# Kernel optimization log

Measured on AMD Instinct MI355X. Metric: run time of the kernel, lower is better.

## Reference

```python
import jax, jax.numpy as jnp
import numpy as np

N = 40000
E = 640000
IN_C = 128
HID = 256
HEADS = 8


def _gat(x, W, att_src, att_dst, bias, src, dst, num_nodes, heads, concat):
    # x: [N, Fin], W: [Fin, heads*C], att_*: [heads, C], bias: [out_dim]
    xp = (x @ W).reshape(num_nodes, heads, -1)          # [N, H, C]
    a_s = jnp.sum(xp * att_src, axis=-1)                # [N, H]
    a_d = jnp.sum(xp * att_dst, axis=-1)                # [N, H]
    e = jax.nn.leaky_relu(a_s[src] + a_d[dst], 0.2)     # [E, H]
    # per-destination-node softmax over incoming edges (self-loops guarantee >=1)
    m = jax.ops.segment_max(e, dst, num_segments=num_nodes)
    m = jnp.where(jnp.isfinite(m), m, 0.0)
    ex = jnp.exp(e - m[dst])
    denom = jax.ops.segment_sum(ex, dst, num_segments=num_nodes)
    alpha = ex / (denom[dst] + 1e-16)                   # [E, H]
    out = jax.ops.segment_sum(xp[src] * alpha[..., None], dst, num_segments=num_nodes)  # [N,H,C]
    out = out.reshape(num_nodes, -1) if concat else out.mean(axis=1)
    return out + bias


def setup_inputs() -> dict:
    key = jax.random.key(0)
    ks = jax.random.split(key, 16)
    C = HID // HEADS
    s = 0.05
    return {
        "x": jax.random.normal(ks[0], (N, IN_C), jnp.float32),
        "edge_index": jax.random.randint(ks[1], (2, E), 0, N, jnp.int32),
        "W0": jax.random.normal(ks[2], (IN_C, HEADS * C), jnp.float32) * s,
        "att_s0": jax.random.normal(ks[3], (HEADS, C), jnp.float32) * s,
        "att_d0": jax.random.normal(ks[4], (HEADS, C), jnp.float32) * s,
        "b0": jnp.zeros((HID,), jnp.float32),
        # BatchNorm(256)
        "gamma0": jnp.ones((HID,), jnp.float32),
        "beta0": jnp.zeros((HID,), jnp.float32),
        # skip projection Linear(128 -> 256)
        "W_skip": jax.random.normal(ks[5], (IN_C, HID), jnp.float32) * s,
        "b_skip": jnp.zeros((HID,), jnp.float32),
        # last layer: GATConv(256 -> 256, heads=1, concat=False)
        "W1": jax.random.normal(ks[6], (HID, HID), jnp.float32) * s,
        "att_s1": jax.random.normal(ks[7], (1, HID), jnp.float32) * s,
        "att_d1": jax.random.normal(ks[8], (1, HID), jnp.float32) * s,
        "b1": jnp.zeros((HID,), jnp.float32),
    }


def reference(x, edge_index, W0, att_s0, att_d0, b0, gamma0, beta0,
              W_skip, b_skip, W1, att_s1, att_d1, b1):
    loops = jnp.arange(N, dtype=edge_index.dtype)
    src = jnp.concatenate([edge_index[0], loops])
    dst = jnp.concatenate([edge_index[1], loops])
    # conv 0 (heads=8, concat)
    h = _gat(x, W0, att_s0, att_d0, b0, src, dst, N, HEADS, True)
    # BatchNorm (training-style batch stats, biased variance, eps=1e-5)
    mu = h.mean(axis=0)
    var = h.var(axis=0)
    h = (h - mu) / jnp.sqrt(var + 1e-5) * gamma0 + beta0
    h = jax.nn.elu(h)
    # dropout is identity in eval mode
    # residual: shapes differ (128 vs 256) -> skip_proj(x_initial) + h at i==0
    h = h + (x @ W_skip + b_skip)
    # conv 1 (heads=1, concat=False -> mean over single head)
    out = _gat(h, W1, att_s1, att_d1, b1, src, dst, N, 1, False)
    return out
```

## Files before the change

kernel.cpp:

```cpp
#include <hip/hip_runtime.h>
#include <hip/hip_bf16.h>

#define NN 40000
#define EE 640000
#define ET 680000
#define MPAD 40064

typedef __attribute__((ext_vector_type(8))) short short8;
typedef __attribute__((ext_vector_type(4))) float f32x4;

__device__ __forceinline__ float bf2f(unsigned u) {
    return __uint_as_float(u << 16);
}
__device__ __forceinline__ unsigned short f2bf(float f) {
    unsigned u = __float_as_uint(f);
    return (unsigned short)((u + 0x7FFFu + ((u >> 16) & 1u)) >> 16);
}
__device__ __forceinline__ void unpack2(unsigned u, float& lo, float& hi) {
    lo = __uint_as_float(u << 16);
    hi = __uint_as_float(u & 0xffff0000u);
}

__global__ __launch_bounds__(256) void conv_x(const float* __restrict__ x,
                                              unsigned short* __restrict__ xb)
{
    int i = blockIdx.x * 256 + threadIdx.x;
    if (i >= MPAD * 128 / 4) return;
    int row = (i * 4) >> 7;
    ushort4 o;
    if (row < NN) {
        float4 v = ((const float4*)x)[i];
        o.x = f2bf(v.x); o.y = f2bf(v.y); o.z = f2bf(v.z); o.w = f2bf(v.w);
    } else { o.x = o.y = o.z = o.w = 0; }
    ((ushort4*)xb)[i] = o;
}

__global__ __launch_bounds__(256) void conv_wt(const float* __restrict__ W,
                                               unsigned short* __restrict__ Wt, int K)
{
    int i = blockIdx.x * 256 + threadIdx.x;
    if (i >= K * 256) return;
    int c = i / K, k = i - c * K;
    Wt[i] = f2bf(W[(size_t)k * 256 + c]);
}

__global__ __launch_bounds__(256) void gemm_bf16(
    const unsigned short* __restrict__ A, const unsigned short* __restrict__ Bt,
    unsigned short* __restrict__ C, int K)
{
    __shared__ unsigned short As[128 * 64];
    int tid = threadIdx.x;
    int rb = blockIdx.x * 128, cb = blockIdx.y * 128;
    int lane = tid & 63, wid = tid >> 6;
    int wm = (wid >> 1) * 64, wn = (wid & 1) * 64;
    int lr = lane & 15, lk = lane >> 4;
    f32x4 acc[4][4] = {};
    for (int kb = 0; kb < K; kb += 64) {
        #pragma unroll
        for (int i = 0; i < 4; i++) {
            int flat = tid + i * 256;
            int r = flat >> 3, c8 = flat & 7;
            int4 v = *(const int4*)(A + (size_t)(rb + r) * K + kb + c8 * 8);
            *(int4*)(&As[r * 64 + ((c8 ^ (r & 7)) * 8)]) = v;
        }
        __syncthreads();
        #pragma unroll
        for (int kk = 0; kk < 2; kk++) {
            int kbase = kb + kk * 32 + lk * 8;
            short8 bfr[4], afr[4];
            #pragma unroll
            for (int n = 0; n < 4; n++)
                bfr[n] = *(const short8*)(Bt + (size_t)(cb + wn + n * 16 + lr) * K + kbase);
            #pragma unroll
            for (int m = 0; m < 4; m++) {
                int row = wm + m * 16 + lr;
                int kchunk = kk * 4 + lk;
                afr[m] = *(const short8*)(&As[row * 64 + ((kchunk ^ (row & 7)) * 8)]);
            }
            #pragma unroll
            for (int m = 0; m < 4; m++)
                #pragma unroll
                for (int n = 0; n < 4; n++)
                    acc[m][n] = __builtin_amdgcn_mfma_f32_16x16x32_bf16(afr[m], bfr[n], acc[m][n], 0, 0, 0);
        }
        __syncthreads();
    }
    #pragma unroll
    for (int m = 0; m < 4; m++)
        #pragma unroll
        for (int n = 0; n < 4; n++) {
            int col = cb + wn + n * 16 + lr;
            #pragma unroll
            for (int j = 0; j < 4; j++) {
                int row = rb + wm + m * 16 + lk * 4 + j;
                C[(size_t)row * 256 + col] = f2bf(acc[m][n][j]);
            }
        }
}

__global__ __launch_bounds__(256) void gemm_skip_bn(
    const unsigned short* __restrict__ A, const unsigned short* __restrict__ Bt,
    const unsigned short* __restrict__ H, unsigned short* __restrict__ Hb,
    const float* __restrict__ gamma, const float* __restrict__ beta,
    const float* __restrict__ bnsum, const float* __restrict__ bnsq,
    const float* __restrict__ bskip, int K)
{
    __shared__ unsigned short As[128 * 64];
    int tid = threadIdx.x;
    int rb = blockIdx.x * 128, cb = blockIdx.y * 128;
    int lane = tid & 63, wid = tid >> 6;
    int wm = (wid >> 1) * 64, wn = (wid & 1) * 64;
    int lr = lane & 15, lk = lane >> 4;
    f32x4 acc[4][4] = {};
    for (int kb = 0; kb < K; kb += 64) {
        #pragma unroll
        for (int i = 0; i < 4; i++) {
            int flat = tid + i * 256;
            int r = flat >> 3, c8 = flat & 7;
            int4 v = *(const int4*)(A + (size_t)(rb + r) * K + kb + c8 * 8);
            *(int4*)(&As[r * 64 + ((c8 ^ (r & 7)) * 8)]) = v;
        }
        __syncthreads();
        #pragma unroll
        for (int kk = 0; kk < 2; kk++) {
            int kbase = kb + kk * 32 + lk * 8;
            short8 bfr[4], afr[4];
            #pragma unroll
            for (int n = 0; n < 4; n++)
                bfr[n] = *(const short8*)(Bt + (size_t)(cb + wn + n * 16 + lr) * K + kbase);
            #pragma unroll
            for (int m = 0; m < 4; m++) {
                int row = wm + m * 16 + lr;
                int kchunk = kk * 4 + lk;
                afr[m] = *(const short8*)(&As[row * 64 + ((kchunk ^ (row & 7)) * 8)]);
            }
            #pragma unroll
            for (int m = 0; m < 4; m++)
                #pragma unroll
                for (int n = 0; n < 4; n++)
                    acc[m][n] = __builtin_amdgcn_mfma_f32_16x16x32_bf16(afr[m], bfr[n], acc[m][n], 0, 0, 0);
        }
        __syncthreads();
    }
    const float invN = 1.0f / (float)NN;
    #pragma unroll
    for (int n = 0; n < 4; n++) {
        int col = cb + wn + n * 16 + lr;
        float mu = bnsum[col] * invN;
        float var = bnsq[col] * invN - mu * mu;
        float inv = rsqrtf(var + 1e-5f) * gamma[col];
        float bet = beta[col], bsk = bskip[col];
        #pragma unroll
        for (int m = 0; m < 4; m++)
            #pragma unroll
            for (int j = 0; j < 4; j++) {
                int row = rb + wm + m * 16 + lk * 4 + j;
                float v = bf2f(H[(size_t)row * 256 + col]);
                float bn = (v - mu) * inv + bet;
                float el = bn > 0.f ? bn : (__expf(bn) - 1.f);
                Hb[(size_t)row * 256 + col] = f2bf(el + acc[m][n][j] + bsk);
            }
    }
}

__global__ __launch_bounds__(256) void csr_count(const int* __restrict__ ei, int* __restrict__ deg)
{
    int e = blockIdx.x * blockDim.x + threadIdx.x;
    if (e >= ET) return;
    int d = (e < EE) ? ei[EE + e] : (e - EE);
    atomicAdd(&deg[d], 1);
}

__global__ __launch_bounds__(1024) void exscan(
    const int* __restrict__ deg, int* __restrict__ rowptr, int* __restrict__ cursor)
{
    __shared__ int wsum[16];
    __shared__ int carry_s;
    int tid = threadIdx.x, lane = tid & 63, wid = tid >> 6;
    if (tid == 0) carry_s = 0;
    __syncthreads();
    for (int base = 0; base < NN; base += 1024) {
        int i = base + tid;
        int v = (i < NN) ? deg[i] : 0;
        int sc = v;
        #pragma unroll
        for (int off = 1; off < 64; off <<= 1) {
            int t = __shfl_up(sc, off);
            if (lane >= off) sc += t;
        }
        if (lane == 63) wsum[wid] = sc;
        __syncthreads();
        if (wid == 0 && lane < 16) {
            int t = wsum[lane];
            #pragma unroll
            for (int off = 1; off < 16; off <<= 1) {
                int u = __shfl_up(t, off);
                if (lane >= off) t += u;
            }
            wsum[lane] = t;
        }
        __syncthreads();
        int carry = carry_s;
        int wpre = wid ? wsum[wid - 1] : 0;
        int excl = carry + wpre + sc - v;
        if (i < NN) { rowptr[i] = excl; cursor[i] = excl; }
        __syncthreads();
        if (tid == 0) carry_s = carry + wsum[15];
    }
    if (tid == 0) rowptr[NN] = carry_s;
}

__global__ __launch_bounds__(256) void csr_fill(
    const int* __restrict__ ei, int* __restrict__ cursor, int* __restrict__ adj)
{
    int e = blockIdx.x * blockDim.x + threadIdx.x;
    if (e >= ET) return;
    int s, d;
    if (e < EE) { s = ei[e]; d = ei[EE + e]; } else { s = d = e - EE; }
    int pos = atomicAdd(&cursor[d], 1);
    adj[pos] = s;
}

__global__ __launch_bounds__(256) void attn_node0(
    const unsigned short* __restrict__ xp, const float* __restrict__ att_s,
    const float* __restrict__ att_d, float* __restrict__ a_s, float* __restrict__ a_d)
{
    int t = blockIdx.x * 256 + threadIdx.x;
    if (t >= NN * 8) return;
    int n = t >> 3, h = t & 7;
    const unsigned short* p = xp + (size_t)n * 256 + h * 32;
    float s = 0.f, dd = 0.f;
    #pragma unroll
    for (int i0 = 0; i0 < 32; i0 += 8) {
        uint4 raw = *(const uint4*)(p + i0);
        unsigned vals[4] = {raw.x, raw.y, raw.z, raw.w};
        #pragma unroll
        for (int q = 0; q < 4; q++) {
            float lo, hi;
            unpack2(vals[q], lo, hi);
            s  += lo * att_s[h * 32 + i0 + q * 2] + hi * att_s[h * 32 + i0 + q * 2 + 1];
            dd += lo * att_d[h * 32 + i0 + q * 2] + hi * att_d[h * 32 + i0 + q * 2 + 1];
        }
    }
    a_s[t] = s; a_d[t] = dd;
}

__global__ __launch_bounds__(256) void attn_node1(
    const unsigned short* __restrict__ xp, const float* __restrict__ att_s,
    const float* __restrict__ att_d, float* __restrict__ a_s, float* __restrict__ a_d)
{
    int w = (blockIdx.x * 256 + threadIdx.x) >> 6;
    int lane = threadIdx.x & 63;
    if (w >= NN) return;
    ushort4 raw = ((const ushort4*)(xp + (size_t)w * 256))[lane];
    float4 a = ((const float4*)att_s)[lane];
    float4 b = ((const float4*)att_d)[lane];
    float v0 = bf2f(raw.x), v1 = bf2f(raw.y), v2 = bf2f(raw.z), v3 = bf2f(raw.w);
    float s  = v0 * a.x + v1 * a.y + v2 * a.z + v3 * a.w;
    float dd = v0 * b.x + v1 * b.y + v2 * b.z + v3 * b.w;
    #pragma unroll
    for (int off = 32; off; off >>= 1) {
        s  += __shfl_down(s, off);
        dd += __shfl_down(dd, off);
    }
    if (lane == 0) { a_s[w] = s; a_d[w] = dd; }
}

__global__ __launch_bounds__(256) void gather0(
    const int* __restrict__ adj, const int* __restrict__ rowptr,
    const unsigned short* __restrict__ xp, const float* __restrict__ a_s,
    const float* __restrict__ a_d, unsigned short* __restrict__ out0)
{
    int w = (blockIdx.x * 256 + threadIdx.x) >> 6;
    int lane = threadIdx.x & 63;
    if (w >= NN) return;
    int h = lane >> 3;
    float ad = a_d[w * 8 + h];
    int p = rowptr[w], end = rowptr[w + 1];
    unsigned loff = (unsigned)lane * 8u;
    float ax0=0,ay0=0,az0=0,aw0=0, ax1=0,ay1=0,az1=0,aw1=0;
    float den0 = 0.f, den1 = 0.f;
    for (; p + 2 <= end; p += 2) {
        int s0 = adj[p], s1 = adj[p + 1];
        float e0 = a_s[s0 * 8 + h] + ad;
        float e1 = a_s[s1 * 8 + h] + ad;
        e0 = fmaxf(e0, 0.2f * e0);
        e1 = fmaxf(e1, 0.2f * e1);
        float w0 = __expf(e0), w1 = __expf(e1);
        uint2 r0 = *(const uint2*)((const char*)xp + ((unsigned)s0 * 512u + loff));
        uint2 r1 = *(const uint2*)((const char*)xp + ((unsigned)s1 * 512u + loff));
        den0 += w0; den1 += w1;
        float lo, hi;
        unpack2(r0.x, lo, hi); ax0 += w0 * lo; ay0 += w0 * hi;
        unpack2(r0.y, lo, hi); az0 += w0 * lo; aw0 += w0 * hi;
        unpack2(r1.x, lo, hi); ax1 += w1 * lo; ay1 += w1 * hi;
        unpack2(r1.y, lo, hi); az1 += w1 * lo; aw1 += w1 * hi;
    }
    if (p < end) {
        int s0 = adj[p];
        float e0 = a_s[s0 * 8 + h] + ad;
        e0 = fmaxf(e0, 0.2f * e0);
        float w0 = __expf(e0);
        uint2 r0 = *(const uint2*)((const char*)xp + ((unsigned)s0 * 512u + loff));
        den0 += w0;
        float lo, hi;
        unpack2(r0.x, lo, hi); ax0 += w0 * lo; ay0 += w0 * hi;
        unpack2(r0.y, lo, hi); az0 += w0 * lo; aw0 += w0 * hi;
    }
    float inv = 1.f / (den0 + den1 + 1e-16f);
    ushort4 o;
    o.x = f2bf((ax0 + ax1) * inv); o.y = f2bf((ay0 + ay1) * inv);
    o.z = f2bf((az0 + az1) * inv); o.w = f2bf((aw0 + aw1) * inv);
    ((ushort4*)(out0 + (size_t)w * 256))[lane] = o;
}

__global__ __launch_bounds__(256) void gather1(
    const int* __restrict__ adj, const int* __restrict__ rowptr,
    const unsigned short* __restrict__ xp, const float* __restrict__ a_s,
    const float* __restrict__ a_d, const float* __restrict__ b1,
    float* __restrict__ out)
{
    int w = (blockIdx.x * 256 + threadIdx.x) >> 6;
    int lane = threadIdx.x & 63;
    if (w >= NN) return;
    float ad = a_d[w];
    int p = rowptr[w], end = rowptr[w + 1];
    unsigned loff = (unsigned)lane * 8u;
    float ax0=0,ay0=0,az0=0,aw0=0, ax1=0,ay1=0,az1=0,aw1=0;
    float den0 = 0.f, den1 = 0.f;
    for (; p + 2 <= end; p += 2) {
        int s0 = adj[p], s1 = adj[p + 1];
        float e0 = a_s[s0] + ad;
        float e1 = a_s[s1] + ad;
        e0 = fmaxf(e0, 0.2f * e0);
        e1 = fmaxf(e1, 0.2f * e1);
        float w0 = __expf(e0), w1 = __expf(e1);
        uint2 r0 = *(const uint2*)((const char*)xp + ((unsigned)s0 * 512u + loff));
        uint2 r1 = *(const uint2*)((const char*)xp + ((unsigned)s1 * 512u + loff));
        den0 += w0; den1 += w1;
        float lo, hi;
        unpack2(r0.x, lo, hi); ax0 += w0 * lo; ay0 += w0 * hi;
        unpack2(r0.y, lo, hi); az0 += w0 * lo; aw0 += w0 * hi;
        unpack2(r1.x, lo, hi); ax1 += w1 * lo; ay1 += w1 * hi;
        unpack2(r1.y, lo, hi); az1 += w1 * lo; aw1 += w1 * hi;
    }
    if (p < end) {
        int s0 = adj[p];
        float e0 = a_s[s0] + ad;
        e0 = fmaxf(e0, 0.2f * e0);
        float w0 = __expf(e0);
        uint2 r0 = *(const uint2*)((const char*)xp + ((unsigned)s0 * 512u + loff));
        den0 += w0;
        float lo, hi;
        unpack2(r0.x, lo, hi); ax0 += w0 * lo; ay0 += w0 * hi;
        unpack2(r0.y, lo, hi); az0 += w0 * lo; aw0 += w0 * hi;
    }
    float inv = 1.f / (den0 + den1 + 1e-16f);
    float4 b = ((const float4*)b1)[lane];
    float4 r = {(ax0 + ax1) * inv + b.x, (ay0 + ay1) * inv + b.y,
                (az0 + az1) * inv + b.z, (aw0 + aw1) * inv + b.w};
    ((float4*)(out + (size_t)w * 256))[lane] = r;
}

__global__ __launch_bounds__(256) void bn_stats(
    const unsigned short* __restrict__ H, float* __restrict__ bnsum, float* __restrict__ bnsq)
{
    int c = threadIdx.x;
    int r0 = blockIdx.x * 64;
    float s = 0.f, sq = 0.f;
    for (int r = r0; r < r0 + 64; r++) {
        float v = bf2f(H[(size_t)r * 256 + c]);
        s += v; sq += v * v;
    }
    atomicAdd(&bnsum[c], s);
    atomicAdd(&bnsq[c], sq);
}

extern "C" void kernel_launch(void* const* d_in, const int* in_sizes, int n_in,
                              void* d_out, int out_size, void* d_ws, size_t ws_size,
                              hipStream_t stream)
{
    const float* x      = (const float*)d_in[0];
    const int*   ei     = (const int*)d_in[1];
    const float* W0     = (const float*)d_in[2];
    const float* att_s0 = (const float*)d_in[3];
    const float* att_d0 = (const float*)d_in[4];
    const float* gamma0 = (const float*)d_in[6];
    const float* beta0  = (const float*)d_in[7];
    const float* W_skip = (const float*)d_in[8];
    const float* b_skip = (const float*)d_in[9];
    const float* W1     = (const float*)d_in[10];
    const float* att_s1 = (const float*)d_in[11];
    const float* att_d1 = (const float*)d_in[12];
    const float* b1     = (const float*)d_in[13];
    float* out = (float*)d_out;

    char* p = (char*)d_ws;
    unsigned short* x_bf  = (unsigned short*)p; p += (size_t)MPAD * 128 * 2;
    unsigned short* xp_bf = (unsigned short*)p; p += (size_t)MPAD * 256 * 2;
    unsigned short* h_bf  = (unsigned short*)p; p += (size_t)MPAD * 256 * 2;
    unsigned short* out0b = (unsigned short*)p; p += (size_t)MPAD * 256 * 2;
    unsigned short* W0t   = (unsigned short*)p; p += (size_t)256 * 128 * 2;
    unsigned short* Wst   = (unsigned short*)p; p += (size_t)256 * 128 * 2;
    unsigned short* W1t   = (unsigned short*)p; p += (size_t)256 * 256 * 2;
    float* a_s   = (float*)p; p += (size_t)NN * 8 * 4;
    float* a_d   = (float*)p; p += (size_t)NN * 8 * 4;
    float* bnsum = (float*)p; p += 256 * 4;
    float* bnsq  = (float*)p; p += 256 * 4;
    int* deg    = (int*)p; p += (size_t)NN * 4;
    int* rowptr = (int*)p; p += (size_t)(NN + 1) * 4;
    int* cursor = (int*)p; p += (size_t)NN * 4;
    int* adj    = (int*)p; p += (size_t)ET * 4;

    hipMemsetAsync(deg, 0, (size_t)NN * 4, stream);
    hipMemsetAsync(bnsum, 0, 512 * 4, stream);
    hipMemsetAsync(out0b + (size_t)NN * 256, 0, (size_t)(MPAD - NN) * 256 * 2, stream);

    conv_x<<<(MPAD * 128 / 4 + 255) / 256, 256, 0, stream>>>(x, x_bf);
    conv_wt<<<(128 * 256 + 255) / 256, 256, 0, stream>>>(W0, W0t, 128);
    conv_wt<<<(128 * 256 + 255) / 256, 256, 0, stream>>>(W_skip, Wst, 128);
    conv_wt<<<(256 * 256 + 255) / 256, 256, 0, stream>>>(W1, W1t, 256);

    csr_count<<<(ET + 255) / 256, 256, 0, stream>>>(ei, deg);
    exscan<<<1, 1024, 0, stream>>>(deg, rowptr, cursor);
    csr_fill<<<(ET + 255) / 256, 256, 0, stream>>>(ei, cursor, adj);

    dim3 gg(MPAD / 128, 2);

    gemm_bf16<<<gg, 256, 0, stream>>>(x_bf, W0t, xp_bf, 128);
    attn_node0<<<(NN * 8 + 255) / 256, 256, 0, stream>>>(xp_bf, att_s0, att_d0, a_s, a_d);
    gather0<<<(NN * 64 + 255) / 256, 256, 0, stream>>>(adj, rowptr, xp_bf, a_s, a_d, out0b);

    bn_stats<<<NN / 64, 256, 0, stream>>>(out0b, bnsum, bnsq);
    gemm_skip_bn<<<gg, 256, 0, stream>>>(x_bf, Wst, out0b, h_bf, gamma0, beta0,
                                         bnsum, bnsq, b_skip, 128);

    gemm_bf16<<<gg, 256, 0, stream>>>(h_bf, W1t, xp_bf, 256);
    attn_node1<<<(NN * 64 + 255) / 256, 256, 0, stream>>>(xp_bf, att_s1, att_d1, a_s, a_d);
    gather1<<<(NN * 64 + 255) / 256, 256, 0, stream>>>(adj, rowptr, xp_bf, a_s, a_d, b1, out);
}
```

Baseline: 342.7 us.

## Fuse skip GEMM into first projection, fold BN stats into gather, exp2 softmax

```diff
diff --git a/kernel.cpp b/kernel.cpp
--- a/kernel.cpp
+++ b/kernel.cpp
@@ -5,6 +5,7 @@
 #define EE 640000
 #define ET 680000
 #define MPAD 40064
+#define LOG2E 1.4426950408889634f
 
 typedef __attribute__((ext_vector_type(8))) short short8;
 typedef __attribute__((ext_vector_type(4))) float f32x4;
@@ -15,6 +16,9 @@
 __device__ __forceinline__ unsigned short f2bf(float f) {
     unsigned u = __float_as_uint(f);
     return (unsigned short)((u + 0x7FFFu + ((u >> 16) & 1u)) >> 16);
+}
+__device__ __forceinline__ unsigned pack2(float lo, float hi) {
+    return ((unsigned)f2bf(lo)) | (((unsigned)f2bf(hi)) << 16);
 }
 __device__ __forceinline__ void unpack2(unsigned u, float& lo, float& hi) {
     lo = __uint_as_float(u << 16);
@@ -45,8 +49,8 @@
 }
 
 __global__ __launch_bounds__(256) void gemm_bf16(
-    const unsigned short* __restrict__ A, const unsigned short* __restrict__ Bt,
-    unsigned short* __restrict__ C, int K)
+    const unsigned short* __restrict__ A, const unsigned short* __restrict__ Btc,
+    unsigned short* __restrict__ C0, unsigned short* __restrict__ C1, int K)
 {
     __shared__ unsigned short As[128 * 64];
     int tid = threadIdx.x;
@@ -70,7 +74,7 @@
             short8 bfr[4], afr[4];
             #pragma unroll
             for (int n = 0; n < 4; n++)
-                bfr[n] = *(const short8*)(Bt + (size_t)(cb + wn + n * 16 + lr) * K + kbase);
+                bfr[n] = *(const short8*)(Btc + (size_t)(cb + wn + n * 16 + lr) * K + kbase);
             #pragma unroll
             for (int m = 0; m < 4; m++) {
                 int row = wm + m * 16 + lr;
@@ -85,82 +89,19 @@
         }
         __syncthreads();
     }
+    unsigned short* C = (cb < 256) ? C0 : C1;
+    int cbase = cb & 255;
     #pragma unroll
     for (int m = 0; m < 4; m++)
         #pragma unroll
         for (int n = 0; n < 4; n++) {
-            int col = cb + wn + n * 16 + lr;
+            int col = cbase + wn + n * 16 + lr;
             #pragma unroll
             for (int j = 0; j < 4; j++) {
                 int row = rb + wm + m * 16 + lk * 4 + j;
                 C[(size_t)row * 256 + col] = f2bf(acc[m][n][j]);
             }
         }
-}
-
-__global__ __launch_bounds__(256) void gemm_skip_bn(
-    const unsigned short* __restrict__ A, const unsigned short* __restrict__ Bt,
-    const unsigned short* __restrict__ H, unsigned short* __restrict__ Hb,
-    const float* __restrict__ gamma, const float* __restrict__ beta,
-    const float* __restrict__ bnsum, const float* __restrict__ bnsq,
-    const float* __restrict__ bskip, int K)
-{
-    __shared__ unsigned short As[128 * 64];
-    int tid = threadIdx.x;
-    int rb = blockIdx.x * 128, cb = blockIdx.y * 128;
-    int lane = tid & 63, wid = tid >> 6;
-    int wm = (wid >> 1) * 64, wn = (wid & 1) * 64;
-    int lr = lane & 15, lk = lane >> 4;
-    f32x4 acc[4][4] = {};
-    for (int kb = 0; kb < K; kb += 64) {
-        #pragma unroll
-        for (int i = 0; i < 4; i++) {
-            int flat = tid + i * 256;
-            int r = flat >> 3, c8 = flat & 7;
-            int4 v = *(const int4*)(A + (size_t)(rb + r) * K + kb + c8 * 8);
-            *(int4*)(&As[r * 64 + ((c8 ^ (r & 7)) * 8)]) = v;
-        }
-        __syncthreads();
-        #pragma unroll
-        for (int kk = 0; kk < 2; kk++) {
-            int kbase = kb + kk * 32 + lk * 8;
-            short8 bfr[4], afr[4];
-            #pragma unroll
-            for (int n = 0; n < 4; n++)
-                bfr[n] = *(const short8*)(Bt + (size_t)(cb + wn + n * 16 + lr) * K + kbase);
-            #pragma unroll
-            for (int m = 0; m < 4; m++) {
-                int row = wm + m * 16 + lr;
-                int kchunk = kk * 4 + lk;
-                afr[m] = *(const short8*)(&As[row * 64 + ((kchunk ^ (row & 7)) * 8)]);
-            }
-            #pragma unroll
-            for (int m = 0; m < 4; m++)
-                #pragma unroll
-                for (int n = 0; n < 4; n++)
-                    acc[m][n] = __builtin_amdgcn_mfma_f32_16x16x32_bf16(afr[m], bfr[n], acc[m][n], 0, 0, 0);
-        }
-        __syncthreads();
-    }
-    const float invN = 1.0f / (float)NN;
-    #pragma unroll
-    for (int n = 0; n < 4; n++) {
-        int col = cb + wn + n * 16 + lr;
-        float mu = bnsum[col] * invN;
-        float var = bnsq[col] * invN - mu * mu;
-        float inv = rsqrtf(var + 1e-5f) * gamma[col];
-        float bet = beta[col], bsk = bskip[col];
-        #pragma unroll
-        for (int m = 0; m < 4; m++)
-            #pragma unroll
-            for (int j = 0; j < 4; j++) {
-                int row = rb + wm + m * 16 + lk * 4 + j;
-                float v = bf2f(H[(size_t)row * 256 + col]);
-                float bn = (v - mu) * inv + bet;
-                float el = bn > 0.f ? bn : (__expf(bn) - 1.f);
-                Hb[(size_t)row * 256 + col] = f2bf(el + acc[m][n][j] + bsk);
-            }
-    }
 }
 
 __global__ __launch_bounds__(256) void csr_count(const int* __restrict__ ei, int* __restrict__ deg)
@@ -242,7 +183,7 @@
             dd += lo * att_d[h * 32 + i0 + q * 2] + hi * att_d[h * 32 + i0 + q * 2 + 1];
         }
     }
-    a_s[t] = s; a_d[t] = dd;
+    a_s[t] = s * LOG2E; a_d[t] = dd * LOG2E;
 }
 
 __global__ __launch_bounds__(256) void attn_node1(
@@ -263,55 +204,129 @@
         s  += __shfl_down(s, off);
         dd += __shfl_down(dd, off);
     }
-    if (lane == 0) { a_s[w] = s; a_d[w] = dd; }
+    if (lane == 0) { a_s[w] = s * LOG2E; a_d[w] = dd * LOG2E; }
 }
 
 __global__ __launch_bounds__(256) void gather0(
     const int* __restrict__ adj, const int* __restrict__ rowptr,
     const unsigned short* __restrict__ xp, const float* __restrict__ a_s,
-    const float* __restrict__ a_d, unsigned short* __restrict__ out0)
-{
-    int w = (blockIdx.x * 256 + threadIdx.x) >> 6;
-    int lane = threadIdx.x & 63;
-    if (w >= NN) return;
-    int h = lane >> 3;
-    float ad = a_d[w * 8 + h];
-    int p = rowptr[w], end = rowptr[w + 1];
-    unsigned loff = (unsigned)lane * 8u;
-    float ax0=0,ay0=0,az0=0,aw0=0, ax1=0,ay1=0,az1=0,aw1=0;
-    float den0 = 0.f, den1 = 0.f;
-    for (; p + 2 <= end; p += 2) {
-        int s0 = adj[p], s1 = adj[p + 1];
-        float e0 = a_s[s0 * 8 + h] + ad;
-        float e1 = a_s[s1 * 8 + h] + ad;
-        e0 = fmaxf(e0, 0.2f * e0);
-        e1 = fmaxf(e1, 0.2f * e1);
-        float w0 = __expf(e0), w1 = __expf(e1);
-        uint2 r0 = *(const uint2*)((const char*)xp + ((unsigned)s0 * 512u + loff));
-        uint2 r1 = *(const uint2*)((const char*)xp + ((unsigned)s1 * 512u + loff));
-        den0 += w0; den1 += w1;
-        float lo, hi;
-        unpack2(r0.x, lo, hi); ax0 += w0 * lo; ay0 += w0 * hi;
-        unpack2(r0.y, lo, hi); az0 += w0 * lo; aw0 += w0 * hi;
-        unpack2(r1.x, lo, hi); ax1 += w1 * lo; ay1 += w1 * hi;
-        unpack2(r1.y, lo, hi); az1 += w1 * lo; aw1 += w1 * hi;
-    }
-    if (p < end) {
-        int s0 = adj[p];
-        float e0 = a_s[s0 * 8 + h] + ad;
-        e0 = fmaxf(e0, 0.2f * e0);
-        float w0 = __expf(e0);
-        uint2 r0 = *(const uint2*)((const char*)xp + ((unsigned)s0 * 512u + loff));
-        den0 += w0;
-        float lo, hi;
-        unpack2(r0.x, lo, hi); ax0 += w0 * lo; ay0 += w0 * hi;
-        unpack2(r0.y, lo, hi); az0 += w0 * lo; aw0 += w0 * hi;
-    }
-    float inv = 1.f / (den0 + den1 + 1e-16f);
-    ushort4 o;
-    o.x = f2bf((ax0 + ax1) * inv); o.y = f2bf((ay0 + ay1) * inv);
-    o.z = f2bf((az0 + az1) * inv); o.w = f2bf((aw0 + aw1) * inv);
-    ((ushort4*)(out0 + (size_t)w * 256))[lane] = o;
+    const float* __restrict__ a_d, unsigned short* __restrict__ out0,
+    float* __restrict__ bnsum, float* __restrict__ bnsq)
+{
+    __shared__ float ls[512];
+    int tid = threadIdx.x;
+    ls[tid] = 0.f; ls[tid + 256] = 0.f;
+    __syncthreads();
+    int w = (blockIdx.x * 256 + tid) >> 6;
+    int lane = tid & 63;
+    if (w < NN) {
+        int h = lane >> 3;
+        float ad = a_d[w * 8 + h];
+        int p = rowptr[w], end = rowptr[w + 1];
+        unsigned loff = (unsigned)lane * 8u;
+        float ax0=0,ay0=0,az0=0,aw0=0, ax1=0,ay1=0,az1=0,aw1=0;
+        float den = 0.f;
+        for (; p + 4 <= end; p += 4) {
+            int s0 = adj[p], s1 = adj[p+1], s2 = adj[p+2], s3 = adj[p+3];
+            float e0 = a_s[s0 * 8 + h] + ad;
+            float e1 = a_s[s1 * 8 + h] + ad;
+            float e2 = a_s[s2 * 8 + h] + ad;
+            float e3 = a_s[s3 * 8 + h] + ad;
+            float w0 = __builtin_amdgcn_exp2f(fmaxf(e0, 0.2f * e0));
+            float w1 = __builtin_amdgcn_exp2f(fmaxf(e1, 0.2f * e1));
+            float w2 = __builtin_amdgcn_exp2f(fmaxf(e2, 0.2f * e2));
+            float w3 = __builtin_amdgcn_exp2f(fmaxf(e3, 0.2f * e3));
+            uint2 r0 = *(const uint2*)((const char*)xp + ((unsigned)s0 * 512u + loff));
+            uint2 r1 = *(const uint2*)((const char*)xp + ((unsigned)s1 * 512u + loff));
+            uint2 r2 = *(const uint2*)((const char*)xp + ((unsigned)s2 * 512u + loff));
+            uint2 r3 = *(const uint2*)((const char*)xp + ((unsigned)s3 * 512u + loff));
+            den += (w0 + w1) + (w2 + w3);
+            float lo, hi;
+            unpack2(r0.x, lo, hi); ax0 += w0 * lo; ay0 += w0 * hi;
+            unpack2(r0.y, lo, hi); az0 += w0 * lo; aw0 += w0 * hi;
+            unpack2(r1.x, lo, hi); ax1 += w1 * lo; ay1 += w1 * hi;
+            unpack2(r1.y, lo, hi); az1 += w1 * lo; aw1 += w1 * hi;
+            unpack2(r2.x, lo, hi); ax0 += w2 * lo; ay0 += w2 * hi;
+            unpack2(r2.y, lo, hi); az0 += w2 * lo; aw0 += w2 * hi;
+            unpack2(r3.x, lo, hi); ax1 += w3 * lo; ay1 += w3 * hi;
+            unpack2(r3.y, lo, hi); az1 += w3 * lo; aw1 += w3 * hi;
+        }
+        for (; p < end; p++) {
+            int s0 = adj[p];
+            float e0 = a_s[s0 * 8 + h] + ad;
+            float w0 = __builtin_amdgcn_exp2f(fmaxf(e0, 0.2f * e0));
+            uint2 r0 = *(const uint2*)((const char*)xp + ((unsigned)s0 * 512u + loff));
+            den += w0;
+            float lo, hi;
+            unpack2(r0.x, lo, hi); ax0 += w0 * lo; ay0 += w0 * hi;
+            unpack2(r0.y, lo, hi); az0 += w0 * lo; aw0 += w0 * hi;
+        }
+        float inv = 1.f / (den + 1e-16f);
+        float vx = (ax0 + ax1) * inv, vy = (ay0 + ay1) * inv;
+        float vz = (az0 + az1) * inv, vw = (aw0 + aw1) * inv;
+        ushort4 o;
+        o.x = f2bf(vx); o.y = f2bf(vy); o.z = f2bf(vz); o.w = f2bf(vw);
+        ((ushort4*)(out0 + (size_t)w * 256))[lane] = o;
+        int c0 = lane * 4;
+        atomicAdd(&ls[c0 + 0], vx); atomicAdd(&ls[256 + c0 + 0], vx * vx);
+        atomicAdd(&ls[c0 + 1], vy); atomicAdd(&ls[256 + c0 + 1], vy * vy);
+        atomicAdd(&ls[c0 + 2], vz); atomicAdd(&ls[256 + c0 + 2], vz * vz);
+        atomicAdd(&ls[c0 + 3], vw); atomicAdd(&ls[256 + c0 + 3], vw * vw);
+    }
+    __syncthreads();
+    atomicAdd(&bnsum[tid], ls[tid]);
+    atomicAdd(&bnsq[tid], ls[tid + 256]);
+}
+
+__global__ __launch_bounds__(256) void bn_coef(
+    const float* __restrict__ bnsum, const float* __restrict__ bnsq,
+    const float* __restrict__ gamma, const float* __restrict__ beta,
+    float* __restrict__ scl, float* __restrict__ sft)
+{
+    int c = threadIdx.x;
+    const float invN = 1.0f / (float)NN;
+    float mu = bnsum[c] * invN;
+    float var = bnsq[c] * invN - mu * mu;
+    float s = rsqrtf(var + 1e-5f) * gamma[c];
+    scl[c] = s;
+    sft[c] = beta[c] - mu * s;
+}
+
+__global__ __launch_bounds__(256) void bn_elu(
+    const unsigned short* __restrict__ out0, unsigned short* __restrict__ hb,
+    const float* __restrict__ scl, const float* __restrict__ sft,
+    const float* __restrict__ bskip)
+{
+    int i = blockIdx.x * 256 + threadIdx.x;
+    if (i >= MPAD * 256 / 8) return;
+    int col0 = (i * 8) & 255;
+    uint4 hv = ((const uint4*)out0)[i];
+    uint4 sv = ((const uint4*)hb)[i];
+    float4 c0 = *(const float4*)(scl + col0);
+    float4 c1 = *(const float4*)(scl + col0 + 4);
+    float4 f0 = *(const float4*)(sft + col0);
+    float4 f1 = *(const float4*)(sft + col0 + 4);
+    float4 k0 = *(const float4*)(bskip + col0);
+    float4 k1 = *(const float4*)(bskip + col0 + 4);
+    float bn[8], sk[8];
+    unpack2(hv.x, bn[0], bn[1]); unpack2(hv.y, bn[2], bn[3]);
+    unpack2(hv.z, bn[4], bn[5]); unpack2(hv.w, bn[6], bn[7]);
+    unpack2(sv.x, sk[0], sk[1]); unpack2(sv.y, sk[2], sk[3]);
+    unpack2(sv.z, sk[4], sk[5]); unpack2(sv.w, sk[6], sk[7]);
+    float cc[8] = {c0.x,c0.y,c0.z,c0.w,c1.x,c1.y,c1.z,c1.w};
+    float ff[8] = {f0.x,f0.y,f0.z,f0.w,f1.x,f1.y,f1.z,f1.w};
+    float kk[8] = {k0.x,k0.y,k0.z,k0.w,k1.x,k1.y,k1.z,k1.w};
+    float r[8];
+    #pragma unroll
+    for (int q = 0; q < 8; q++) {
+        float b = bn[q] * cc[q] + ff[q];
+        float el = b > 0.f ? b : (__expf(b) - 1.f);
+        r[q] = el + sk[q] + kk[q];
+    }
+    uint4 o;
+    o.x = pack2(r[0], r[1]); o.y = pack2(r[2], r[3]);
+    o.z = pack2(r[4], r[5]); o.w = pack2(r[6], r[7]);
+    ((uint4*)hb)[i] = o;
 }
 
 __global__ __launch_bounds__(256) void gather1(
@@ -327,53 +342,47 @@
     int p = rowptr[w], end = rowptr[w + 1];
     unsigned loff = (unsigned)lane * 8u;
     float ax0=0,ay0=0,az0=0,aw0=0, ax1=0,ay1=0,az1=0,aw1=0;
-    float den0 = 0.f, den1 = 0.f;
-    for (; p + 2 <= end; p += 2) {
-        int s0 = adj[p], s1 = adj[p + 1];
+    float den = 0.f;
+    for (; p + 4 <= end; p += 4) {
+        int s0 = adj[p], s1 = adj[p+1], s2 = adj[p+2], s3 = adj[p+3];
         float e0 = a_s[s0] + ad;
         float e1 = a_s[s1] + ad;
-        e0 = fmaxf(e0, 0.2f * e0);
-        e1 = fmaxf(e1, 0.2f * e1);
-        float w0 = __expf(e0), w1 = __expf(e1);
+        float e2 = a_s[s2] + ad;
+        float e3 = a_s[s3] + ad;
+        float w0 = __builtin_amdgcn_exp2f(fmaxf(e0, 0.2f * e0));
+        float w1 = __builtin_amdgcn_exp2f(fmaxf(e1, 0.2f * e1));
+        float w2 = __builtin_amdgcn_exp2f(fmaxf(e2, 0.2f * e2));
+        float w3 = __builtin_amdgcn_exp2f(fmaxf(e3, 0.2f * e3));
         uint2 r0 = *(const uint2*)((const char*)xp + ((unsigned)s0 * 512u + loff));
         uint2 r1 = *(const uint2*)((const char*)xp + ((unsigned)s1 * 512u + loff));
-        den0 += w0; den1 += w1;
+        uint2 r2 = *(const uint2*)((const char*)xp + ((unsigned)s2 * 512u + loff));
+        uint2 r3 = *(const uint2*)((const char*)xp + ((unsigned)s3 * 512u + loff));
+        den += (w0 + w1) + (w2 + w3);
         float lo, hi;
         unpack2(r0.x, lo, hi); ax0 += w0 * lo; ay0 += w0 * hi;
         unpack2(r0.y, lo, hi); az0 += w0 * lo; aw0 += w0 * hi;
         unpack2(r1.x, lo, hi); ax1 += w1 * lo; ay1 += w1 * hi;
         unpack2(r1.y, lo, hi); az1 += w1 * lo; aw1 += w1 * hi;
-    }
-    if (p < end) {
+        unpack2(r2.x, lo, hi); ax0 += w2 * lo; ay0 += w2 * hi;
+        unpack2(r2.y, lo, hi); az0 += w2 * lo; aw0 += w2 * hi;
+        unpack2(r3.x, lo, hi); ax1 += w3 * lo; ay1 += w3 * hi;
+        unpack2(r3.y, lo, hi); az1 += w3 * lo; aw1 += w3 * hi;
+    }
+    for (; p < end; p++) {
         int s0 = adj[p];
         float e0 = a_s[s0] + ad;
-        e0 = fmaxf(e0, 0.2f * e0);
-        float w0 = __expf(e0);
+        float w0 = __builtin_amdgcn_exp2f(fmaxf(e0, 0.2f * e0));
         uint2 r0 = *(const uint2*)((const char*)xp + ((unsigned)s0 * 512u + loff));
-        den0 += w0;
+        den += w0;
         float lo, hi;
         unpack2(r0.x, lo, hi); ax0 += w0 * lo; ay0 += w0 * hi;
         unpack2(r0.y, lo, hi); az0 += w0 * lo; aw0 += w0 * hi;
     }
-    float inv = 1.f / (den0 + den1 + 1e-16f);
+    float inv = 1.f / (den + 1e-16f);
     float4 b = ((const float4*)b1)[lane];
     float4 r = {(ax0 + ax1) * inv + b.x, (ay0 + ay1) * inv + b.y,
                 (az0 + az1) * inv + b.z, (aw0 + aw1) * inv + b.w};
     ((float4*)(out + (size_t)w * 256))[lane] = r;
-}
-
-__global__ __launch_bounds__(256) void bn_stats(
-    const unsigned short* __restrict__ H, float* __restrict__ bnsum, float* __restrict__ bnsq)
-{
-    int c = threadIdx.x;
-    int r0 = blockIdx.x * 64;
-    float s = 0.f, sq = 0.f;
-    for (int r = r0; r < r0 + 64; r++) {
-        float v = bf2f(H[(size_t)r * 256 + c]);
-        s += v; sq += v * v;
-    }
-    atomicAdd(&bnsum[c], s);
-    atomicAdd(&bnsq[c], sq);
 }
 
 extern "C" void kernel_launch(void* const* d_in, const int* in_sizes, int n_in,
@@ -400,13 +409,14 @@
     unsigned short* xp_bf = (unsigned short*)p; p += (size_t)MPAD * 256 * 2;
     unsigned short* h_bf  = (unsigned short*)p; p += (size_t)MPAD * 256 * 2;
     unsigned short* out0b = (unsigned short*)p; p += (size_t)MPAD * 256 * 2;
-    unsigned short* W0t   = (unsigned short*)p; p += (size_t)256 * 128 * 2;
-    unsigned short* Wst   = (unsigned short*)p; p += (size_t)256 * 128 * 2;
+    unsigned short* Wtc   = (unsigned short*)p; p += (size_t)512 * 128 * 2;
     unsigned short* W1t   = (unsigned short*)p; p += (size_t)256 * 256 * 2;
     float* a_s   = (float*)p; p += (size_t)NN * 8 * 4;
     float* a_d   = (float*)p; p += (size_t)NN * 8 * 4;
     float* bnsum = (float*)p; p += 256 * 4;
     float* bnsq  = (float*)p; p += 256 * 4;
+    float* scl   = (float*)p; p += 256 * 4;
+    float* sft   = (float*)p; p += 256 * 4;
     int* deg    = (int*)p; p += (size_t)NN * 4;
     int* rowptr = (int*)p; p += (size_t)(NN + 1) * 4;
     int* cursor = (int*)p; p += (size_t)NN * 4;
@@ -417,25 +427,25 @@
     hipMemsetAsync(out0b + (size_t)NN * 256, 0, (size_t)(MPAD - NN) * 256 * 2, stream);
 
     conv_x<<<(MPAD * 128 / 4 + 255) / 256, 256, 0, stream>>>(x, x_bf);
-    conv_wt<<<(128 * 256 + 255) / 256, 256, 0, stream>>>(W0, W0t, 128);
-    conv_wt<<<(128 * 256 + 255) / 256, 256, 0, stream>>>(W_skip, Wst, 128);
+    conv_wt<<<(128 * 256 + 255) / 256, 256, 0, stream>>>(W0, Wtc, 128);
+    conv_wt<<<(128 * 256 + 255) / 256, 256, 0, stream>>>(W_skip, Wtc + 256 * 128, 128);
     conv_wt<<<(256 * 256 + 255) / 256, 256, 0, stream>>>(W1, W1t, 256);
 
     csr_count<<<(ET + 255) / 256, 256, 0, stream>>>(ei, deg);
     exscan<<<1, 1024, 0, stream>>>(deg, rowptr, cursor);
     csr_fill<<<(ET + 255) / 256, 256, 0, stream>>>(ei, cursor, adj);
 
-    dim3 gg(MPAD / 128, 2);
-
-    gemm_bf16<<<gg, 256, 0, stream>>>(x_bf, W0t, xp_bf, 128);
+    dim3 gg0(MPAD / 128, 4);
+    gemm_bf16<<<gg0, 256, 0, stream>>>(x_bf, Wtc, xp_bf, h_bf, 128);
     attn_node0<<<(NN * 8 + 255) / 256, 256, 0, stream>>>(xp_bf, att_s0, att_d0, a_s, a_d);
-    gather0<<<(NN * 64 + 255) / 256, 256, 0, stream>>>(adj, rowptr, xp_bf, a_s, a_d, out0b);
-
-    bn_stats<<<NN / 64, 256, 0, stream>>>(out0b, bnsum, bnsq);
-    gemm_skip_bn<<<gg, 256, 0, stream>>>(x_bf, Wst, out0b, h_bf, gamma0, beta0,
-                                         bnsum, bnsq, b_skip, 128);
-
-    gemm_bf16<<<gg, 256, 0, stream>>>(h_bf, W1t, xp_bf, 256);
+    gather0<<<(NN * 64 + 255) / 256, 256, 0, stream>>>(adj, rowptr, xp_bf, a_s, a_d,
+                                                       out0b, bnsum, bnsq);
+
+    bn_coef<<<1, 256, 0, stream>>>(bnsum, bnsq, gamma0, beta0, scl, sft);
+    bn_elu<<<(MPAD * 256 / 8 + 255) / 256, 256, 0, stream>>>(out0b, h_bf, scl, sft, b_skip);
+
+    dim3 gg1(MPAD / 128, 2);
+    gemm_bf16<<<gg1, 256, 0, stream>>>(h_bf, W1t, xp_bf, xp_bf, 256);
     attn_node1<<<(NN * 64 + 255) / 256, 256, 0, stream>>>(xp_bf, att_s1, att_d1, a_s, a_d);
     gather1<<<(NN * 64 + 255) / 256, 256, 0, stream>>>(adj, rowptr, xp_bf, a_s, a_d, b1, out);
 }
```

New measurement: 530.5 us. 54.8% more time.
